# Kernel optimization log

Hardware: AMD Instinct MI355X
Metric: run time of the kernel (lower is better)

Reference implementation:

```python
import jax, jax.numpy as jnp
import numpy as np
from jax import lax


def _bilinear_sample(u, py, px):
    # u: [B,C,H,W]; py,px: [B,K,H,W] fractional coords; zero outside bounds
    H, W = u.shape[2], u.shape[3]
    y0 = jnp.floor(py)
    x0 = jnp.floor(px)
    y0i = y0.astype(jnp.int32)
    x0i = x0.astype(jnp.int32)
    wy1 = py - y0
    wy0 = 1.0 - wy1
    wx1 = px - x0
    wx0 = 1.0 - wx1

    def corner(yi, xi, w):
        valid = (yi >= 0) & (yi < H) & (xi >= 0) & (xi < W)
        yc = jnp.clip(yi, 0, H - 1)
        xc = jnp.clip(xi, 0, W - 1)
        # per-batch fancy gather: ub[:, y, x] -> [C,K,H,W]
        g = jax.vmap(lambda ub, y, x: ub[:, y, x])(u, yc, xc)  # [B,C,K,H,W]
        return g * (w * valid)[:, None]

    return (corner(y0i, x0i, wy0 * wx0)
            + corner(y0i, x0i + 1, wy0 * wx1)
            + corner(y0i + 1, x0i, wy1 * wx0)
            + corner(y0i + 1, x0i + 1, wy1 * wx1))


def _fam_forward(x, u, weight, bias, offset_w, offset_b):
    k = weight.shape[-1]
    pad = k // 2
    K = k * k
    B, C, H, W = u.shape
    # offset-predicting conv on concat(x, u), SAME padding
    concat = jnp.concatenate([x, u], axis=1)
    offset = lax.conv_general_dilated(concat, offset_w, (1, 1), [(pad, pad), (pad, pad)])
    offset = offset + offset_b[None, :, None, None]  # [B, 2K, H, W]
    off = offset.reshape(B, K, 2, H, W)
    dy = off[:, :, 0]
    dx = off[:, :, 1]
    ft = offset.dtype
    ki = jnp.arange(k, dtype=ft)
    ky = jnp.repeat(ki, k)  # [K] kernel row offsets
    kx = jnp.tile(ki, k)    # [K] kernel col offsets
    py = jnp.arange(H, dtype=ft)[None, None, :, None] - pad + ky[None, :, None, None] + dy
    px = jnp.arange(W, dtype=ft)[None, None, None, :] - pad + kx[None, :, None, None] + dx
    sampled = _bilinear_sample(u, py, px)  # [B,C,K,H,W]
    w = weight.reshape(weight.shape[0], weight.shape[1], K)  # [O,C,K]
    return jnp.einsum('bckhw,ock->bohw', sampled, w) + bias[None, :, None, None]


def setup_inputs() -> dict:
    key = jax.random.key(0)
    ks = jax.random.split(key, 4)
    B, Cx, Cu, H, W, k = 8, 128, 128, 64, 64, 3
    x = jax.random.normal(ks[0], (B, Cx, H, W), jnp.float32)
    u = jax.random.normal(ks[1], (B, Cu, H, W), jnp.float32)
    fan_in = Cu * k * k  # kaiming_uniform a=1 -> bound = sqrt(3/fan_in)
    bound = float(np.sqrt(3.0 / fan_in))
    weight = jax.random.uniform(ks[2], (Cu, Cu, k, k), jnp.float32, -bound, bound)
    bias = jnp.zeros((Cu,), jnp.float32)
    offset_w = jax.random.normal(ks[3], (2 * k * k, Cx + Cu, k, k), jnp.float32) * 0.01
    offset_b = jnp.zeros((2 * k * k,), jnp.float32)
    return {"x": x, "u": u, "weight": weight, "bias": bias,
            "offset_w": offset_w, "offset_b": offset_b}


def reference(x, u, weight, bias, offset_w, offset_b):
    return _fam_forward(x, u, weight, bias, offset_w, offset_b)
```

## Files before the change

kernel.cpp:

```cpp
#include <hip/hip_runtime.h>

#define BB 8
#define CC 128
#define HH 64
#define WW 64
#define NOFF 18

typedef __bf16 bf16x8 __attribute__((ext_vector_type(8)));
typedef float  f32x4  __attribute__((ext_vector_type(4)));
typedef float  f32x2u __attribute__((ext_vector_type(2), aligned(4)));

__global__ __launch_bounds__(256) void prep_kernel(
    const float* __restrict__ w, const float* __restrict__ ow,
    __bf16* __restrict__ af, __bf16* __restrict__ waf)
{
    int idx = blockIdx.x * 256 + threadIdx.x;
    if (idx < 147456) {
        int j    = idx & 7;
        int lane = (idx >> 3) & 63;
        int ks   = (idx >> 9) & 3;
        int mt2  = (idx >> 11) & 7;
        int k    = idx >> 14;
        int o = mt2 * 16 + (lane & 15);
        int c = ks * 32 + (lane >> 4) * 8 + j;
        af[idx] = (__bf16)w[(o * CC + c) * 9 + k];
    } else if (idx < 147456 + 73728) {
        int t    = idx - 147456;
        int j    = t & 7;
        int lane = (t >> 3) & 63;
        int ks   = (t >> 9) & 7;
        int mt   = (t >> 12) & 1;
        int kk   = t >> 13;
        int oc = mt * 16 + (lane & 15);
        int ic = ks * 32 + (lane >> 4) * 8 + j;
        float v = (oc < NOFF) ? ow[(oc * 256 + ic) * 9 + kk] : 0.f;
        waf[t] = (__bf16)v;
    }
}

__global__ __launch_bounds__(256) void transpose_kernel(
    const float* __restrict__ x, const float* __restrict__ u,
    __bf16* __restrict__ ct)
{
    const int id   = blockIdx.x;
    const int b    = id & 7;
    const int y    = id >> 3;
    const int tid  = threadIdx.x;
    const int lane = tid & 63;
    const int wv   = tid >> 6;

    __shared__ __align__(16) __bf16 t[64][264];

#pragma unroll
    for (int g = 0; g < 8; ++g) {
        bf16x8 pk;
#pragma unroll
        for (int j = 0; j < 8; ++j) {
            int ic = wv * 64 + g * 8 + j;
            float v = (ic < CC)
                ? x[((size_t)(b * CC + ic) * HH + y) * WW + lane]
                : u[((size_t)(b * CC + (ic - CC)) * HH + y) * WW + lane];
            pk[j] = (__bf16)v;
        }
        *(bf16x8*)&t[lane][wv * 64 + g * 8] = pk;
    }
    __syncthreads();

    __bf16* dst = ct + (size_t)(b * HH + y) * WW * 256;
#pragma unroll
    for (int p = 0; p < 8; ++p) {
        int idx = p * 256 + tid;
        int px = idx >> 5, ch = idx & 31;
        *(bf16x8*)(dst + px * 256 + ch * 8) = *(const bf16x8*)&t[px][ch * 8];
    }
}

#define TS 264
__global__ __launch_bounds__(256) void offset_conv_fast_kernel(
    const __bf16* __restrict__ ct, const __bf16* __restrict__ waf,
    const float* __restrict__ ob, float* __restrict__ off)
{
    const int id   = blockIdx.x;
    const int b    = id & 7;
    const int h    = id >> 3;
    const int tid  = threadIdx.x;
    const int lane = tid & 63;
    const int wv   = tid >> 6;
    const int col  = lane & 15;
    const int quad = lane >> 4;

    __shared__ __align__(16) __bf16 T[66][TS];
    {
        int ic = tid;
        T[0][ic]  = (__bf16)0.f;
        T[65][ic] = (__bf16)0.f;
    }

    f32x4 acc0 = {0.f, 0.f, 0.f, 0.f};
    f32x4 acc1 = {0.f, 0.f, 0.f, 0.f};
    const bf16x8* wafp = (const bf16x8*)waf;

    for (int kh = 0; kh < 3; ++kh) {
        int y = h - 1 + kh;
        if (y < 0 || y >= HH) continue;
        __syncthreads();
        const __bf16* row = ct + (size_t)(b * HH + y) * WW * 256;
#pragma unroll
        for (int p = 0; p < 8; ++p) {
            int idx = p * 256 + tid;
            int px = idx >> 5, ch = idx & 31;
            *(bf16x8*)&T[px + 1][ch * 8] = *(const bf16x8*)(row + px * 256 + ch * 8);
        }
        __syncthreads();

#pragma unroll
        for (int kw = 0; kw < 3; ++kw) {
            int kk = kh * 3 + kw;
            const __bf16* brow = &T[wv * 16 + col + kw][quad * 8];
#pragma unroll
            for (int ks = 0; ks < 8; ++ks) {
                bf16x8 bfrag = *(const bf16x8*)(brow + ks * 32);
                bf16x8 a0 = wafp[((kk * 2 + 0) * 8 + ks) * 64 + lane];
                bf16x8 a1 = wafp[((kk * 2 + 1) * 8 + ks) * 64 + lane];
                acc0 = __builtin_amdgcn_mfma_f32_16x16x32_bf16(a0, bfrag, acc0, 0, 0, 0);
                acc1 = __builtin_amdgcn_mfma_f32_16x16x32_bf16(a1, bfrag, acc1, 0, 0, 0);
            }
        }
    }

    int w2 = wv * 16 + col;
#pragma unroll
    for (int r = 0; r < 4; ++r) {
        int oc = quad * 4 + r;
        off[((size_t)(b * NOFF + oc) * HH + h) * WW + w2] = acc0[r] + ob[oc];
    }
#pragma unroll
    for (int r = 0; r < 4; ++r) {
        int oc = 16 + quad * 4 + r;
        if (oc < NOFF)
            off[((size_t)(b * NOFF + oc) * HH + h) * WW + w2] = acc1[r] + ob[oc];
    }
}

__global__ __launch_bounds__(256) void fam_main_fast_kernel(
    const __bf16* __restrict__ ct, const __bf16* __restrict__ af,
    const float* __restrict__ bias, const float* __restrict__ off,
    float* __restrict__ out)
{
    const int id   = blockIdx.x;
    const int b    = id & 7;
    const int h    = id >> 3;
    const int tid  = threadIdx.x;
    const int lane = tid & 63;
    const int wv   = tid >> 6;
    const int col  = lane & 15;
    const int quad = lane >> 4;

    __shared__ __align__(16) __bf16 sampT[64][136];
    __shared__ float s_ax[9][64], s_ay[9][64], s_bx[9][64], s_by[9][64];
    __shared__ int   s_i0[9][64], s_i1[9][64];

    for (int t = tid; t < 9 * 64; t += 256) {
        int k  = t >> 6;
        int wq = t & 63;
        float dy = off[((size_t)(b * NOFF + 2 * k)     * HH + h) * WW + wq];
        float dx = off[((size_t)(b * NOFF + 2 * k + 1) * HH + h) * WW + wq];
        float py = (float)(h - 1 + k / 3) + dy;
        float px = (float)(wq - 1 + k % 3) + dx;
        float y0f = floorf(py), x0f = floorf(px);
        int y0 = (int)y0f, x0 = (int)x0f;
        float fy = py - y0f, fx = px - x0f;
        bool vy0 = (y0 >= 0) && (y0 < HH);
        bool vy1 = (y0 + 1 >= 0) && (y0 + 1 < HH);
        bool vx0 = (x0 >= 0) && (x0 < WW);
        bool vx1 = (x0 + 1 >= 0) && (x0 + 1 < WW);
        float w00 = (1.f - fy) * (1.f - fx) * ((vy0 && vx0) ? 1.f : 0.f);
        float w01 = (1.f - fy) * fx         * ((vy0 && vx1) ? 1.f : 0.f);
        float w10 = fy * (1.f - fx)         * ((vy1 && vx0) ? 1.f : 0.f);
        float w11 = fy * fx                 * ((vy1 && vx1) ? 1.f : 0.f);
        int y0c = min(max(y0, 0), HH - 1);
        int y1c = min(max(y0 + 1, 0), HH - 1);
        int x0c = min(max(x0, 0), WW - 1);
        int x1c = min(max(x0 + 1, 0), WW - 1);
        int xl  = min(max(x0, 0), WW - 2);
        float ax = ((x0c == xl)     ? w00 : 0.f) + ((x1c == xl)     ? w01 : 0.f);
        float ay = ((x0c == xl + 1) ? w00 : 0.f) + ((x1c == xl + 1) ? w01 : 0.f);
        float bx = ((x0c == xl)     ? w10 : 0.f) + ((x1c == xl)     ? w11 : 0.f);
        float by = ((x0c == xl + 1) ? w10 : 0.f) + ((x1c == xl + 1) ? w11 : 0.f);
        s_ax[k][wq] = ax; s_ay[k][wq] = ay;
        s_bx[k][wq] = bx; s_by[k][wq] = by;
        s_i0[k][wq] = y0c * WW + xl;
        s_i1[k][wq] = y1c * WW + xl;
    }
    __syncthreads();

    f32x4 acc[2][4];
#pragma unroll
    for (int mt = 0; mt < 2; ++mt)
#pragma unroll
        for (int nt = 0; nt < 4; ++nt) acc[mt][nt] = (f32x4){0.f, 0.f, 0.f, 0.f};

    const __bf16* ctb = ct + (size_t)b * (HH * WW * 256);
    const bf16x8* afp = (const bf16x8*)af;

    for (int k = 0; k < 9; ++k) {
#pragma unroll
        for (int p = 0; p < 4; ++p) {
            int idx = p * 256 + tid;
            int px = idx >> 4, ch = idx & 15;
            float ax = s_ax[k][px], ay = s_ay[k][px];
            float bx = s_bx[k][px], by = s_by[k][px];
            const __bf16* r0 = ctb + (size_t)s_i0[k][px] * 256 + 128 + ch * 8;
            const __bf16* r1 = ctb + (size_t)s_i1[k][px] * 256 + 128 + ch * 8;
            bf16x8 A  = *(const bf16x8*)r0;
            bf16x8 Bv = *(const bf16x8*)(r0 + 256);
            bf16x8 Cv = *(const bf16x8*)r1;
            bf16x8 Dv = *(const bf16x8*)(r1 + 256);
            bf16x8 res;
#pragma unroll
            for (int j = 0; j < 8; ++j)
                res[j] = (__bf16)(ax * (float)A[j] + ay * (float)Bv[j] +
                                  bx * (float)Cv[j] + by * (float)Dv[j]);
            *(bf16x8*)&sampT[px][ch * 8] = res;
        }
        __syncthreads();

#pragma unroll
        for (int ks = 0; ks < 4; ++ks) {
            bf16x8 a0 = afp[((k * 8 + wv * 2 + 0) * 4 + ks) * 64 + lane];
            bf16x8 a1 = afp[((k * 8 + wv * 2 + 1) * 4 + ks) * 64 + lane];
            int crow = ks * 32 + quad * 8;
#pragma unroll
            for (int nt = 0; nt < 4; ++nt) {
                bf16x8 bfrag = *(const bf16x8*)&sampT[nt * 16 + col][crow];
                acc[0][nt] = __builtin_amdgcn_mfma_f32_16x16x32_bf16(
                    a0, bfrag, acc[0][nt], 0, 0, 0);
                acc[1][nt] = __builtin_amdgcn_mfma_f32_16x16x32_bf16(
                    a1, bfrag, acc[1][nt], 0, 0, 0);
            }
        }
        __syncthreads();
    }

#pragma unroll
    for (int mt = 0; mt < 2; ++mt) {
#pragma unroll
        for (int r = 0; r < 4; ++r) {
            int o = wv * 32 + mt * 16 + quad * 4 + r;
            float bv = bias[o];
#pragma unroll
            for (int nt = 0; nt < 4; ++nt)
                out[((size_t)(b * CC + o) * HH + h) * WW + nt * 16 + col] =
                    acc[mt][nt][r] + bv;
        }
    }
}

__global__ __launch_bounds__(256) void offset_conv_mfma_kernel(
    const float* __restrict__ x, const float* __restrict__ u,
    const __bf16* __restrict__ waf, const float* __restrict__ ob,
    float* __restrict__ off)
{
    const int id   = blockIdx.x;
    const int b    = id & 7;
    const int h    = id >> 3;
    const int tid  = threadIdx.x;
    const int lane = tid & 63;
    const int wv   = tid >> 6;
    const int col  = lane & 15;
    const int quad = lane >> 4;

    __shared__ __align__(16) __bf16 T[66][TS];
    {
        int ic = tid;
        T[0][ic]  = (__bf16)0.f;
        T[65][ic] = (__bf16)0.f;
    }

    f32x4 acc0 = {0.f, 0.f, 0.f, 0.f};
    f32x4 acc1 = {0.f, 0.f, 0.f, 0.f};
    const bf16x8* wafp = (const bf16x8*)waf;

    for (int kh = 0; kh < 3; ++kh) {
        int y = h - 1 + kh;
        if (y < 0 || y >= HH) continue;
        __syncthreads();
        {
            int w2 = lane;
#pragma unroll
            for (int g = 0; g < 8; ++g) {
                bf16x8 pk;
#pragma unroll
                for (int j = 0; j < 8; ++j) {
                    int ic = wv * 64 + g * 8 + j;
                    float v = (ic < CC)
                        ? x[((size_t)(b * CC + ic) * HH + y) * WW + w2]
                        : u[((size_t)(b * CC + (ic - CC)) * HH + y) * WW + w2];
                    pk[j] = (__bf16)v;
                }
                *(bf16x8*)&T[w2 + 1][wv * 64 + g * 8] = pk;
            }
        }
        __syncthreads();

#pragma unroll
        for (int kw = 0; kw < 3; ++kw) {
            int kk = kh * 3 + kw;
            const __bf16* brow = &T[wv * 16 + col + kw][quad * 8];
#pragma unroll
            for (int ks = 0; ks < 8; ++ks) {
                bf16x8 bfrag = *(const bf16x8*)(brow + ks * 32);
                bf16x8 a0 = wafp[((kk * 2 + 0) * 8 + ks) * 64 + lane];
                bf16x8 a1 = wafp[((kk * 2 + 1) * 8 + ks) * 64 + lane];
                acc0 = __builtin_amdgcn_mfma_f32_16x16x32_bf16(a0, bfrag, acc0, 0, 0, 0);
                acc1 = __builtin_amdgcn_mfma_f32_16x16x32_bf16(a1, bfrag, acc1, 0, 0, 0);
            }
        }
    }

    int w2 = wv * 16 + col;
#pragma unroll
    for (int r = 0; r < 4; ++r) {
        int oc = quad * 4 + r;
        off[((size_t)(b * NOFF + oc) * HH + h) * WW + w2] = acc0[r] + ob[oc];
    }
#pragma unroll
    for (int r = 0; r < 4; ++r) {
        int oc = 16 + quad * 4 + r;
        if (oc < NOFF)
            off[((size_t)(b * NOFF + oc) * HH + h) * WW + w2] = acc1[r] + ob[oc];
    }
}

__global__ __launch_bounds__(256) void fam_main_kernel(
    const float* __restrict__ u, const __bf16* __restrict__ af,
    const float* __restrict__ bias, const float* __restrict__ off,
    float* __restrict__ out)
{
    const int id   = blockIdx.x;
    const int b    = id & 7;
    const int h    = id >> 3;
    const int tid  = threadIdx.x;
    const int lane = tid & 63;
    const int wv   = tid >> 6;
    const int col  = lane & 15;
    const int quad = lane >> 4;

    __shared__ __align__(16) __bf16 sampT[64][136];
    __shared__ float s_ax[9][64], s_ay[9][64], s_bx[9][64], s_by[9][64];
    __shared__ int   s_i0[9][64], s_i1[9][64];

    for (int t = tid; t < 9 * 64; t += 256) {
        int k  = t >> 6;
        int wq = t & 63;
        float dy = off[((size_t)(b * NOFF + 2 * k)     * HH + h) * WW + wq];
        float dx = off[((size_t)(b * NOFF + 2 * k + 1) * HH + h) * WW + wq];
        float py = (float)(h - 1 + k / 3) + dy;
        float px = (float)(wq - 1 + k % 3) + dx;
        float y0f = floorf(py), x0f = floorf(px);
        int y0 = (int)y0f, x0 = (int)x0f;
        float fy = py - y0f, fx = px - x0f;
        bool vy0 = (y0 >= 0) && (y0 < HH);
        bool vy1 = (y0 + 1 >= 0) && (y0 + 1 < HH);
        bool vx0 = (x0 >= 0) && (x0 < WW);
        bool vx1 = (x0 + 1 >= 0) && (x0 + 1 < WW);
        float w00 = (1.f - fy) * (1.f - fx) * ((vy0 && vx0) ? 1.f : 0.f);
        float w01 = (1.f - fy) * fx         * ((vy0 && vx1) ? 1.f : 0.f);
        float w10 = fy * (1.f - fx)         * ((vy1 && vx0) ? 1.f : 0.f);
        float w11 = fy * fx                 * ((vy1 && vx1) ? 1.f : 0.f);
        int y0c = min(max(y0, 0), HH - 1);
        int y1c = min(max(y0 + 1, 0), HH - 1);
        int x0c = min(max(x0, 0), WW - 1);
        int x1c = min(max(x0 + 1, 0), WW - 1);
        int xl  = min(max(x0, 0), WW - 2);
        float ax = ((x0c == xl)     ? w00 : 0.f) + ((x1c == xl)     ? w01 : 0.f);
        float ay = ((x0c == xl + 1) ? w00 : 0.f) + ((x1c == xl + 1) ? w01 : 0.f);
        float bx = ((x0c == xl)     ? w10 : 0.f) + ((x1c == xl)     ? w11 : 0.f);
        float by = ((x0c == xl + 1) ? w10 : 0.f) + ((x1c == xl + 1) ? w11 : 0.f);
        s_ax[k][wq] = ax; s_ay[k][wq] = ay;
        s_bx[k][wq] = bx; s_by[k][wq] = by;
        s_i0[k][wq] = y0c * WW + xl;
        s_i1[k][wq] = y1c * WW + xl;
    }
    __syncthreads();

    f32x4 acc[2][4];
#pragma unroll
    for (int mt = 0; mt < 2; ++mt)
#pragma unroll
        for (int nt = 0; nt < 4; ++nt) acc[mt][nt] = (f32x4){0.f, 0.f, 0.f, 0.f};

    const float* ub = u + (size_t)b * (CC * HH * WW);
    const bf16x8* afp = (const bf16x8*)af;

    for (int k = 0; k < 9; ++k) {
        {
            float ax = s_ax[k][lane], ay = s_ay[k][lane];
            float bx = s_bx[k][lane], by = s_by[k][lane];
            int   i0 = s_i0[k][lane], i1 = s_i1[k][lane];
#pragma unroll 4
            for (int g = 0; g < 4; ++g) {
                bf16x8 pk;
#pragma unroll
                for (int j = 0; j < 8; ++j) {
                    const float* up = ub + (size_t)(wv * 32 + g * 8 + j) * (HH * WW);
                    f32x2u r0 = *(const f32x2u*)(up + i0);
                    f32x2u r1 = *(const f32x2u*)(up + i1);
                    float v = ax * r0.x + ay * r0.y + bx * r1.x + by * r1.y;
                    pk[j] = (__bf16)v;
                }
                *(bf16x8*)&sampT[lane][wv * 32 + g * 8] = pk;
            }
        }
        __syncthreads();

#pragma unroll
        for (int ks = 0; ks < 4; ++ks) {
            bf16x8 a0 = afp[((k * 8 + wv * 2 + 0) * 4 + ks) * 64 + lane];
            bf16x8 a1 = afp[((k * 8 + wv * 2 + 1) * 4 + ks) * 64 + lane];
            int crow = ks * 32 + quad * 8;
#pragma unroll
            for (int nt = 0; nt < 4; ++nt) {
                bf16x8 bfrag = *(const bf16x8*)&sampT[nt * 16 + col][crow];
                acc[0][nt] = __builtin_amdgcn_mfma_f32_16x16x32_bf16(
                    a0, bfrag, acc[0][nt], 0, 0, 0);
                acc[1][nt] = __builtin_amdgcn_mfma_f32_16x16x32_bf16(
                    a1, bfrag, acc[1][nt], 0, 0, 0);
            }
        }
        __syncthreads();
    }

#pragma unroll
    for (int mt = 0; mt < 2; ++mt) {
#pragma unroll
        for (int r = 0; r < 4; ++r) {
            int o = wv * 32 + mt * 16 + quad * 4 + r;
            float bv = bias[o];
#pragma unroll
            for (int nt = 0; nt < 4; ++nt)
                out[((size_t)(b * CC + o) * HH + h) * WW + nt * 16 + col] =
                    acc[mt][nt][r] + bv;
        }
    }
}

extern "C" void kernel_launch(void* const* d_in, const int* in_sizes, int n_in,
                              void* d_out, int out_size, void* d_ws, size_t ws_size,
                              hipStream_t stream) {
    const float* x    = (const float*)d_in[0];
    const float* u    = (const float*)d_in[1];
    const float* wgt  = (const float*)d_in[2];
    const float* bias = (const float*)d_in[3];
    const float* ow   = (const float*)d_in[4];
    const float* ob   = (const float*)d_in[5];
    float* out = (float*)d_out;

    float*  off = (float*)d_ws;
    __bf16* af  = (__bf16*)(off + (size_t)BB * NOFF * HH * WW);
    __bf16* waf = af + 147456;
    __bf16* ct  = waf + 73728;
    const size_t need_fast = 2359296 + 294912 + 147456 + (size_t)BB * HH * WW * 256 * 2;

    hipLaunchKernelGGL(prep_kernel, dim3(864), dim3(256), 0, stream,
                       wgt, ow, af, waf);

    if (ws_size >= need_fast) {
        hipLaunchKernelGGL(transpose_kernel, dim3(512), dim3(256), 0, stream,
                           x, u, ct);
        hipLaunchKernelGGL(offset_conv_fast_kernel, dim3(512), dim3(256), 0, stream,
                           ct, waf, ob, off);
        hipLaunchKernelGGL(fam_main_fast_kernel, dim3(512), dim3(256), 0, stream,
                           ct, af, bias, off, out);
    } else {
        hipLaunchKernelGGL(offset_conv_mfma_kernel, dim3(512), dim3(256), 0, stream,
                           x, u, waf, ob, off);
        hipLaunchKernelGGL(fam_main_kernel, dim3(512), dim3(256), 0, stream,
                           u, af, bias, off, out);
    }
}
```

Measured before the change: 137.3 us.

## Fuse offset conv into main deformable kernel and merge prep with transpose

New measurement: 129.8 us. -5.5%, faster.

```diff
diff --git a/kernel.cpp b/kernel.cpp
--- a/kernel.cpp
+++ b/kernel.cpp
@@ -9,6 +9,260 @@
 typedef __bf16 bf16x8 __attribute__((ext_vector_type(8)));
 typedef float  f32x4  __attribute__((ext_vector_type(4)));
 typedef float  f32x2u __attribute__((ext_vector_type(2), aligned(4)));
+
+__global__ __launch_bounds__(256) void prep_transpose_kernel(
+    const float* __restrict__ x, const float* __restrict__ u,
+    const float* __restrict__ w, const float* __restrict__ ow,
+    __bf16* __restrict__ ct, __bf16* __restrict__ af, __bf16* __restrict__ waf)
+{
+    const int tid = threadIdx.x;
+    if (blockIdx.x < 512) {
+        const int id   = blockIdx.x;
+        const int b    = id & 7;
+        const int y    = id >> 3;
+        const int lane = tid & 63;
+        const int wv   = tid >> 6;
+
+        __shared__ __align__(16) __bf16 t[64][264];
+#pragma unroll
+        for (int g = 0; g < 8; ++g) {
+            bf16x8 pk;
+#pragma unroll
+            for (int j = 0; j < 8; ++j) {
+                int ic = wv * 64 + g * 8 + j;
+                float v = (ic < CC)
+                    ? x[((size_t)(b * CC + ic) * HH + y) * WW + lane]
+                    : u[((size_t)(b * CC + (ic - CC)) * HH + y) * WW + lane];
+                pk[j] = (__bf16)v;
+            }
+            *(bf16x8*)&t[lane][wv * 64 + g * 8] = pk;
+        }
+        __syncthreads();
+
+        __bf16* dst = ct + (size_t)(b * HH + y) * WW * 256;
+#pragma unroll
+        for (int p = 0; p < 8; ++p) {
+            int idx = p * 256 + tid;
+            int px = idx >> 5, ch = idx & 31;
+            *(bf16x8*)(dst + px * 256 + ch * 8) = *(const bf16x8*)&t[px][ch * 8];
+        }
+    } else {
+        int idx = (blockIdx.x - 512) * 256 + tid;
+        if (idx < 147456) {
+            int j    = idx & 7;
+            int lane = (idx >> 3) & 63;
+            int ks   = (idx >> 9) & 3;
+            int mt2  = (idx >> 11) & 7;
+            int k    = idx >> 14;
+            int o = mt2 * 16 + (lane & 15);
+            int c = ks * 32 + (lane >> 4) * 8 + j;
+            af[idx] = (__bf16)w[(o * CC + c) * 9 + k];
+        } else if (idx < 147456 + 73728) {
+            int t2   = idx - 147456;
+            int j    = t2 & 7;
+            int lane = (t2 >> 3) & 63;
+            int ks   = (t2 >> 9) & 7;
+            int mt   = (t2 >> 12) & 1;
+            int kk   = t2 >> 13;
+            int oc = mt * 16 + (lane & 15);
+            int ic = ks * 32 + (lane >> 4) * 8 + j;
+            float v = (oc < NOFF) ? ow[(oc * 256 + ic) * 9 + kk] : 0.f;
+            waf[t2] = (__bf16)v;
+        }
+    }
+}
+
+__global__ __launch_bounds__(256, 2) void fam_fused_kernel(
+    const __bf16* __restrict__ ct, const __bf16* __restrict__ waf,
+    const __bf16* __restrict__ af, const float* __restrict__ ob,
+    const float* __restrict__ bias, float* __restrict__ out)
+{
+    const int id   = blockIdx.x;
+    const int b    = id & 7;
+    const int h    = id >> 3;
+    const int tid  = threadIdx.x;
+    const int lane = tid & 63;
+    const int wv   = tid >> 6;
+    const int col  = lane & 15;
+    const int quad = lane >> 4;
+
+    __shared__ __align__(16) unsigned char smem[48640];
+    __shared__ float off_lds[NOFF][64];
+
+    __bf16 (*T)[264] = (__bf16(*)[264])smem;
+    __bf16 (*sampT)[64][136] = (__bf16(*)[64][136])smem;
+    float* s_ax = (float*)(smem + 34816);
+    float* s_ay = s_ax + 576;
+    float* s_bx = s_ay + 576;
+    float* s_by = s_bx + 576;
+    int*   s_i0 = (int*)(s_by + 576);
+    int*   s_i1 = s_i0 + 576;
+
+    {
+        T[0][tid]  = (__bf16)0.f;
+        T[65][tid] = (__bf16)0.f;
+
+        f32x4 acc0 = {0.f, 0.f, 0.f, 0.f};
+        f32x4 acc1 = {0.f, 0.f, 0.f, 0.f};
+        const bf16x8* wafp = (const bf16x8*)waf;
+
+        for (int kh = 0; kh < 3; ++kh) {
+            int y = h - 1 + kh;
+            if (y < 0 || y >= HH) continue;
+            __syncthreads();
+            const __bf16* row = ct + (size_t)(b * HH + y) * WW * 256;
+#pragma unroll
+            for (int p = 0; p < 8; ++p) {
+                int idx = p * 256 + tid;
+                int px = idx >> 5, ch = idx & 31;
+                *(bf16x8*)&T[px + 1][ch * 8] =
+                    *(const bf16x8*)(row + px * 256 + ch * 8);
+            }
+            __syncthreads();
+
+#pragma unroll
+            for (int kw = 0; kw < 3; ++kw) {
+                int kk = kh * 3 + kw;
+                const __bf16* brow = &T[wv * 16 + col + kw][quad * 8];
+#pragma unroll
+                for (int ks = 0; ks < 8; ++ks) {
+                    bf16x8 bfrag = *(const bf16x8*)(brow + ks * 32);
+                    bf16x8 a0 = wafp[((kk * 2 + 0) * 8 + ks) * 64 + lane];
+                    bf16x8 a1 = wafp[((kk * 2 + 1) * 8 + ks) * 64 + lane];
+                    acc0 = __builtin_amdgcn_mfma_f32_16x16x32_bf16(a0, bfrag, acc0, 0, 0, 0);
+                    acc1 = __builtin_amdgcn_mfma_f32_16x16x32_bf16(a1, bfrag, acc1, 0, 0, 0);
+                }
+            }
+        }
+
+        int w2 = wv * 16 + col;
+#pragma unroll
+        for (int r = 0; r < 4; ++r)
+            off_lds[quad * 4 + r][w2] = acc0[r] + ob[quad * 4 + r];
+#pragma unroll
+        for (int r = 0; r < 4; ++r) {
+            int oc = 16 + quad * 4 + r;
+            if (oc < NOFF) off_lds[oc][w2] = acc1[r] + ob[oc];
+        }
+    }
+    __syncthreads();
+
+    for (int t = tid; t < 9 * 64; t += 256) {
+        int k  = t >> 6;
+        int wq = t & 63;
+        float dy = off_lds[2 * k][wq];
+        float dx = off_lds[2 * k + 1][wq];
+        float py = (float)(h - 1 + k / 3) + dy;
+        float px = (float)(wq - 1 + k % 3) + dx;
+        float y0f = floorf(py), x0f = floorf(px);
+        int y0 = (int)y0f, x0 = (int)x0f;
+        float fy = py - y0f, fx = px - x0f;
+        bool vy0 = (y0 >= 0) && (y0 < HH);
+        bool vy1 = (y0 + 1 >= 0) && (y0 + 1 < HH);
+        bool vx0 = (x0 >= 0) && (x0 < WW);
+        bool vx1 = (x0 + 1 >= 0) && (x0 + 1 < WW);
+        float w00 = (1.f - fy) * (1.f - fx) * ((vy0 && vx0) ? 1.f : 0.f);
+        float w01 = (1.f - fy) * fx         * ((vy0 && vx1) ? 1.f : 0.f);
+        float w10 = fy * (1.f - fx)         * ((vy1 && vx0) ? 1.f : 0.f);
+        float w11 = fy * fx                 * ((vy1 && vx1) ? 1.f : 0.f);
+        int y0c = min(max(y0, 0), HH - 1);
+        int y1c = min(max(y0 + 1, 0), HH - 1);
+        int x0c = min(max(x0, 0), WW - 1);
+        int x1c = min(max(x0 + 1, 0), WW - 1);
+        int xl  = min(max(x0, 0), WW - 2);
+        float ax = ((x0c == xl)     ? w00 : 0.f) + ((x1c == xl)     ? w01 : 0.f);
+        float ay = ((x0c == xl + 1) ? w00 : 0.f) + ((x1c == xl + 1) ? w01 : 0.f);
+        float bx = ((x0c == xl)     ? w10 : 0.f) + ((x1c == xl)     ? w11 : 0.f);
+        float by = ((x0c == xl + 1) ? w10 : 0.f) + ((x1c == xl + 1) ? w11 : 0.f);
+        s_ax[k * 64 + wq] = ax; s_ay[k * 64 + wq] = ay;
+        s_bx[k * 64 + wq] = bx; s_by[k * 64 + wq] = by;
+        s_i0[k * 64 + wq] = y0c * WW + xl;
+        s_i1[k * 64 + wq] = y1c * WW + xl;
+    }
+    __syncthreads();
+
+    f32x4 acc[2][4];
+#pragma unroll
+    for (int mt = 0; mt < 2; ++mt)
+#pragma unroll
+        for (int nt = 0; nt < 4; ++nt) acc[mt][nt] = (f32x4){0.f, 0.f, 0.f, 0.f};
+
+    const __bf16* ctb = ct + (size_t)b * (HH * WW * 256);
+    const bf16x8* afp = (const bf16x8*)af;
+
+    bf16x8 rA[4], rB[4], rC[4], rD[4];
+
+    auto preload = [&](int kk) {
+#pragma unroll
+        for (int p = 0; p < 4; ++p) {
+            int idx = p * 256 + tid;
+            int px = idx >> 4, ch = idx & 15;
+            const __bf16* r0 = ctb + (size_t)s_i0[kk * 64 + px] * 256 + 128 + ch * 8;
+            const __bf16* r1 = ctb + (size_t)s_i1[kk * 64 + px] * 256 + 128 + ch * 8;
+            rA[p] = *(const bf16x8*)r0;
+            rB[p] = *(const bf16x8*)(r0 + 256);
+            rC[p] = *(const bf16x8*)r1;
+            rD[p] = *(const bf16x8*)(r1 + 256);
+        }
+    };
+    auto combine = [&](int kk, int buf) {
+#pragma unroll
+        for (int p = 0; p < 4; ++p) {
+            int idx = p * 256 + tid;
+            int px = idx >> 4, ch = idx & 15;
+            float ax = s_ax[kk * 64 + px], ay = s_ay[kk * 64 + px];
+            float bx = s_bx[kk * 64 + px], by = s_by[kk * 64 + px];
+            bf16x8 res;
+#pragma unroll
+            for (int j = 0; j < 8; ++j)
+                res[j] = (__bf16)(ax * (float)rA[p][j] + ay * (float)rB[p][j] +
+                                  bx * (float)rC[p][j] + by * (float)rD[p][j]);
+            *(bf16x8*)&sampT[buf][px][ch * 8] = res;
+        }
+    };
+    auto domfma = [&](int kk, int buf) {
+#pragma unroll
+        for (int ks = 0; ks < 4; ++ks) {
+            bf16x8 a0 = afp[((kk * 8 + wv * 2 + 0) * 4 + ks) * 64 + lane];
+            bf16x8 a1 = afp[((kk * 8 + wv * 2 + 1) * 4 + ks) * 64 + lane];
+            int crow = ks * 32 + quad * 8;
+#pragma unroll
+            for (int nt = 0; nt < 4; ++nt) {
+                bf16x8 bfrag = *(const bf16x8*)&sampT[buf][nt * 16 + col][crow];
+                acc[0][nt] = __builtin_amdgcn_mfma_f32_16x16x32_bf16(
+                    a0, bfrag, acc[0][nt], 0, 0, 0);
+                acc[1][nt] = __builtin_amdgcn_mfma_f32_16x16x32_bf16(
+                    a1, bfrag, acc[1][nt], 0, 0, 0);
+            }
+        }
+    };
+
+    preload(0);
+    combine(0, 0);
+    preload(1);
+    __syncthreads();
+    for (int k = 0; k < 9; ++k) {
+        domfma(k, k & 1);
+        if (k < 8) {
+            combine(k + 1, (k + 1) & 1);
+            if (k + 2 <= 8) preload(k + 2);
+            __syncthreads();
+        }
+    }
+
+#pragma unroll
+    for (int mt = 0; mt < 2; ++mt) {
+#pragma unroll
+        for (int r = 0; r < 4; ++r) {
+            int o = wv * 32 + mt * 16 + quad * 4 + r;
+            float bv = bias[o];
+#pragma unroll
+            for (int nt = 0; nt < 4; ++nt)
+                out[((size_t)(b * CC + o) * HH + h) * WW + nt * 16 + col] =
+                    acc[mt][nt][r] + bv;
+        }
+    }
+}
 
 __global__ __launch_bounds__(256) void prep_kernel(
     const float* __restrict__ w, const float* __restrict__ ow,
@@ -38,47 +292,11 @@
     }
 }
 
-__global__ __launch_bounds__(256) void transpose_kernel(
+#define TS 264
+__global__ __launch_bounds__(256) void offset_conv_mfma_kernel(
     const float* __restrict__ x, const float* __restrict__ u,
-    __bf16* __restrict__ ct)
-{
-    const int id   = blockIdx.x;
-    const int b    = id & 7;
-    const int y    = id >> 3;
-    const int tid  = threadIdx.x;
-    const int lane = tid & 63;
-    const int wv   = tid >> 6;
-
-    __shared__ __align__(16) __bf16 t[64][264];
-
-#pragma unroll
-    for (int g = 0; g < 8; ++g) {
-        bf16x8 pk;
-#pragma unroll
-        for (int j = 0; j < 8; ++j) {
-            int ic = wv * 64 + g * 8 + j;
-            float v = (ic < CC)
-                ? x[((size_t)(b * CC + ic) * HH + y) * WW + lane]
-                : u[((size_t)(b * CC + (ic - CC)) * HH + y) * WW + lane];
-            pk[j] = (__bf16)v;
-        }
-        *(bf16x8*)&t[lane][wv * 64 + g * 8] = pk;
-    }
-    __syncthreads();
-
-    __bf16* dst = ct + (size_t)(b * HH + y) * WW * 256;
-#pragma unroll
-    for (int p = 0; p < 8; ++p) {
-        int idx = p * 256 + tid;
-        int px = idx >> 5, ch = idx & 31;
-        *(bf16x8*)(dst + px * 256 + ch * 8) = *(const bf16x8*)&t[px][ch * 8];
-    }
-}
-
-#define TS 264
-__global__ __launch_bounds__(256) void offset_conv_fast_kernel(
-    const __bf16* __restrict__ ct, const __bf16* __restrict__ waf,
-    const float* __restrict__ ob, float* __restrict__ off)
+    const __bf16* __restrict__ waf, const float* __restrict__ ob,
+    float* __restrict__ off)
 {
     const int id   = blockIdx.x;
     const int b    = id & 7;
@@ -91,9 +309,8 @@
 
     __shared__ __align__(16) __bf16 T[66][TS];
     {
-        int ic = tid;
-        T[0][ic]  = (__bf16)0.f;
-        T[65][ic] = (__bf16)0.f;
+        T[0][tid]  = (__bf16)0.f;
+        T[65][tid] = (__bf16)0.f;
     }
 
     f32x4 acc0 = {0.f, 0.f, 0.f, 0.f};
@@ -104,12 +321,21 @@
         int y = h - 1 + kh;
         if (y < 0 || y >= HH) continue;
         __syncthreads();
-        const __bf16* row = ct + (size_t)(b * HH + y) * WW * 256;
-#pragma unroll
-        for (int p = 0; p < 8; ++p) {
-            int idx = p * 256 + tid;
-            int px = idx >> 5, ch = idx & 31;
-            *(bf16x8*)&T[px + 1][ch * 8] = *(const bf16x8*)(row + px * 256 + ch * 8);
+        {
+            int w2 = lane;
+#pragma unroll
+            for (int g = 0; g < 8; ++g) {
+                bf16x8 pk;
+#pragma unroll
+                for (int j = 0; j < 8; ++j) {
+                    int ic = wv * 64 + g * 8 + j;
+                    float v = (ic < CC)
+                        ? x[((size_t)(b * CC + ic) * HH + y) * WW + w2]
+                        : u[((size_t)(b * CC + (ic - CC)) * HH + y) * WW + w2];
+                    pk[j] = (__bf16)v;
+                }
+                *(bf16x8*)&T[w2 + 1][wv * 64 + g * 8] = pk;
+            }
         }
         __syncthreads();
 
@@ -142,8 +368,8 @@
     }
 }
 
-__global__ __launch_bounds__(256) void fam_main_fast_kernel(
-    const __bf16* __restrict__ ct, const __bf16* __restrict__ af,
+__global__ __launch_bounds__(256) void fam_main_kernel(
+    const float* __restrict__ u, const __bf16* __restrict__ af,
     const float* __restrict__ bias, const float* __restrict__ off,
     float* __restrict__ out)
 {
@@ -200,196 +426,6 @@
 #pragma unroll
         for (int nt = 0; nt < 4; ++nt) acc[mt][nt] = (f32x4){0.f, 0.f, 0.f, 0.f};
 
-    const __bf16* ctb = ct + (size_t)b * (HH * WW * 256);
-    const bf16x8* afp = (const bf16x8*)af;
-
-    for (int k = 0; k < 9; ++k) {
-#pragma unroll
-        for (int p = 0; p < 4; ++p) {
-            int idx = p * 256 + tid;
-            int px = idx >> 4, ch = idx & 15;
-            float ax = s_ax[k][px], ay = s_ay[k][px];
-            float bx = s_bx[k][px], by = s_by[k][px];
-            const __bf16* r0 = ctb + (size_t)s_i0[k][px] * 256 + 128 + ch * 8;
-            const __bf16* r1 = ctb + (size_t)s_i1[k][px] * 256 + 128 + ch * 8;
-            bf16x8 A  = *(const bf16x8*)r0;
-            bf16x8 Bv = *(const bf16x8*)(r0 + 256);
-            bf16x8 Cv = *(const bf16x8*)r1;
-            bf16x8 Dv = *(const bf16x8*)(r1 + 256);
-            bf16x8 res;
-#pragma unroll
-            for (int j = 0; j < 8; ++j)
-                res[j] = (__bf16)(ax * (float)A[j] + ay * (float)Bv[j] +
-                                  bx * (float)Cv[j] + by * (float)Dv[j]);
-            *(bf16x8*)&sampT[px][ch * 8] = res;
-        }
-        __syncthreads();
-
-#pragma unroll
-        for (int ks = 0; ks < 4; ++ks) {
-            bf16x8 a0 = afp[((k * 8 + wv * 2 + 0) * 4 + ks) * 64 + lane];
-            bf16x8 a1 = afp[((k * 8 + wv * 2 + 1) * 4 + ks) * 64 + lane];
-            int crow = ks * 32 + quad * 8;
-#pragma unroll
-            for (int nt = 0; nt < 4; ++nt) {
-                bf16x8 bfrag = *(const bf16x8*)&sampT[nt * 16 + col][crow];
-                acc[0][nt] = __builtin_amdgcn_mfma_f32_16x16x32_bf16(
-                    a0, bfrag, acc[0][nt], 0, 0, 0);
-                acc[1][nt] = __builtin_amdgcn_mfma_f32_16x16x32_bf16(
-                    a1, bfrag, acc[1][nt], 0, 0, 0);
-            }
-        }
-        __syncthreads();
-    }
-
-#pragma unroll
-    for (int mt = 0; mt < 2; ++mt) {
-#pragma unroll
-        for (int r = 0; r < 4; ++r) {
-            int o = wv * 32 + mt * 16 + quad * 4 + r;
-            float bv = bias[o];
-#pragma unroll
-            for (int nt = 0; nt < 4; ++nt)
-                out[((size_t)(b * CC + o) * HH + h) * WW + nt * 16 + col] =
-                    acc[mt][nt][r] + bv;
-        }
-    }
-}
-
-__global__ __launch_bounds__(256) void offset_conv_mfma_kernel(
-    const float* __restrict__ x, const float* __restrict__ u,
-    const __bf16* __restrict__ waf, const float* __restrict__ ob,
-    float* __restrict__ off)
-{
-    const int id   = blockIdx.x;
-    const int b    = id & 7;
-    const int h    = id >> 3;
-    const int tid  = threadIdx.x;
-    const int lane = tid & 63;
-    const int wv   = tid >> 6;
-    const int col  = lane & 15;
-    const int quad = lane >> 4;
-
-    __shared__ __align__(16) __bf16 T[66][TS];
-    {
-        int ic = tid;
-        T[0][ic]  = (__bf16)0.f;
-        T[65][ic] = (__bf16)0.f;
-    }
-
-    f32x4 acc0 = {0.f, 0.f, 0.f, 0.f};
-    f32x4 acc1 = {0.f, 0.f, 0.f, 0.f};
-    const bf16x8* wafp = (const bf16x8*)waf;
-
-    for (int kh = 0; kh < 3; ++kh) {
-        int y = h - 1 + kh;
-        if (y < 0 || y >= HH) continue;
-        __syncthreads();
-        {
-            int w2 = lane;
-#pragma unroll
-            for (int g = 0; g < 8; ++g) {
-                bf16x8 pk;
-#pragma unroll
-                for (int j = 0; j < 8; ++j) {
-                    int ic = wv * 64 + g * 8 + j;
-                    float v = (ic < CC)
-                        ? x[((size_t)(b * CC + ic) * HH + y) * WW + w2]
-                        : u[((size_t)(b * CC + (ic - CC)) * HH + y) * WW + w2];
-                    pk[j] = (__bf16)v;
-                }
-                *(bf16x8*)&T[w2 + 1][wv * 64 + g * 8] = pk;
-            }
-        }
-        __syncthreads();
-
-#pragma unroll
-        for (int kw = 0; kw < 3; ++kw) {
-            int kk = kh * 3 + kw;
-            const __bf16* brow = &T[wv * 16 + col + kw][quad * 8];
-#pragma unroll
-            for (int ks = 0; ks < 8; ++ks) {
-                bf16x8 bfrag = *(const bf16x8*)(brow + ks * 32);
-                bf16x8 a0 = wafp[((kk * 2 + 0) * 8 + ks) * 64 + lane];
-                bf16x8 a1 = wafp[((kk * 2 + 1) * 8 + ks) * 64 + lane];
-                acc0 = __builtin_amdgcn_mfma_f32_16x16x32_bf16(a0, bfrag, acc0, 0, 0, 0);
-                acc1 = __builtin_amdgcn_mfma_f32_16x16x32_bf16(a1, bfrag, acc1, 0, 0, 0);
-            }
-        }
-    }
-
-    int w2 = wv * 16 + col;
-#pragma unroll
-    for (int r = 0; r < 4; ++r) {
-        int oc = quad * 4 + r;
-        off[((size_t)(b * NOFF + oc) * HH + h) * WW + w2] = acc0[r] + ob[oc];
-    }
-#pragma unroll
-    for (int r = 0; r < 4; ++r) {
-        int oc = 16 + quad * 4 + r;
-        if (oc < NOFF)
-            off[((size_t)(b * NOFF + oc) * HH + h) * WW + w2] = acc1[r] + ob[oc];
-    }
-}
-
-__global__ __launch_bounds__(256) void fam_main_kernel(
-    const float* __restrict__ u, const __bf16* __restrict__ af,
-    const float* __restrict__ bias, const float* __restrict__ off,
-    float* __restrict__ out)
-{
-    const int id   = blockIdx.x;
-    const int b    = id & 7;
-    const int h    = id >> 3;
-    const int tid  = threadIdx.x;
-    const int lane = tid & 63;
-    const int wv   = tid >> 6;
-    const int col  = lane & 15;
-    const int quad = lane >> 4;
-
-    __shared__ __align__(16) __bf16 sampT[64][136];
-    __shared__ float s_ax[9][64], s_ay[9][64], s_bx[9][64], s_by[9][64];
-    __shared__ int   s_i0[9][64], s_i1[9][64];
-
-    for (int t = tid; t < 9 * 64; t += 256) {
-        int k  = t >> 6;
-        int wq = t & 63;
-        float dy = off[((size_t)(b * NOFF + 2 * k)     * HH + h) * WW + wq];
-        float dx = off[((size_t)(b * NOFF + 2 * k + 1) * HH + h) * WW + wq];
-        float py = (float)(h - 1 + k / 3) + dy;
-        float px = (float)(wq - 1 + k % 3) + dx;
-        float y0f = floorf(py), x0f = floorf(px);
-        int y0 = (int)y0f, x0 = (int)x0f;
-        float fy = py - y0f, fx = px - x0f;
-        bool vy0 = (y0 >= 0) && (y0 < HH);
-        bool vy1 = (y0 + 1 >= 0) && (y0 + 1 < HH);
-        bool vx0 = (x0 >= 0) && (x0 < WW);
-        bool vx1 = (x0 + 1 >= 0) && (x0 + 1 < WW);
-        float w00 = (1.f - fy) * (1.f - fx) * ((vy0 && vx0) ? 1.f : 0.f);
-        float w01 = (1.f - fy) * fx         * ((vy0 && vx1) ? 1.f : 0.f);
-        float w10 = fy * (1.f - fx)         * ((vy1 && vx0) ? 1.f : 0.f);
-        float w11 = fy * fx                 * ((vy1 && vx1) ? 1.f : 0.f);
-        int y0c = min(max(y0, 0), HH - 1);
-        int y1c = min(max(y0 + 1, 0), HH - 1);
-        int x0c = min(max(x0, 0), WW - 1);
-        int x1c = min(max(x0 + 1, 0), WW - 1);
-        int xl  = min(max(x0, 0), WW - 2);
-        float ax = ((x0c == xl)     ? w00 : 0.f) + ((x1c == xl)     ? w01 : 0.f);
-        float ay = ((x0c == xl + 1) ? w00 : 0.f) + ((x1c == xl + 1) ? w01 : 0.f);
-        float bx = ((x0c == xl)     ? w10 : 0.f) + ((x1c == xl)     ? w11 : 0.f);
-        float by = ((x0c == xl + 1) ? w10 : 0.f) + ((x1c == xl + 1) ? w11 : 0.f);
-        s_ax[k][wq] = ax; s_ay[k][wq] = ay;
-        s_bx[k][wq] = bx; s_by[k][wq] = by;
-        s_i0[k][wq] = y0c * WW + xl;
-        s_i1[k][wq] = y1c * WW + xl;
-    }
-    __syncthreads();
-
-    f32x4 acc[2][4];
-#pragma unroll
-    for (int mt = 0; mt < 2; ++mt)
-#pragma unroll
-        for (int nt = 0; nt < 4; ++nt) acc[mt][nt] = (f32x4){0.f, 0.f, 0.f, 0.f};
-
     const float* ub = u + (size_t)b * (CC * HH * WW);
     const bf16x8* afp = (const bf16x8*)af;
 
@@ -462,17 +498,14 @@
     __bf16* ct  = waf + 73728;
     const size_t need_fast = 2359296 + 294912 + 147456 + (size_t)BB * HH * WW * 256 * 2;
 
-    hipLaunchKernelGGL(prep_kernel, dim3(864), dim3(256), 0, stream,
-                       wgt, ow, af, waf);
-
     if (ws_size >= need_fast) {
-        hipLaunchKernelGGL(transpose_kernel, dim3(512), dim3(256), 0, stream,
-                           x, u, ct);
-        hipLaunchKernelGGL(offset_conv_fast_kernel, dim3(512), dim3(256), 0, stream,
-                           ct, waf, ob, off);
-        hipLaunchKernelGGL(fam_main_fast_kernel, dim3(512), dim3(256), 0, stream,
-                           ct, af, bias, off, out);
+        hipLaunchKernelGGL(prep_transpose_kernel, dim3(1376), dim3(256), 0, stream,
+                           x, u, wgt, ow, ct, af, waf);
+        hipLaunchKernelGGL(fam_fused_kernel, dim3(512), dim3(256), 0, stream,
+                           ct, waf, af, ob, bias, out);
     } else {
+        hipLaunchKernelGGL(prep_kernel, dim3(864), dim3(256), 0, stream,
+                           wgt, ow, af, waf);
         hipLaunchKernelGGL(offset_conv_mfma_kernel, dim3(512), dim3(256), 0, stream,
                            x, u, waf, ob, off);
         hipLaunchKernelGGL(fam_main_kernel, dim3(512), dim3(256), 0, stream,
```
